# Kernel tuning notes

Hardware: AMD Instinct MI355X
Metric: run time of the kernel (lower is better)

## Reference

```python
import jax, jax.numpy as jnp
import numpy as np

L_OUTPUT = 1024  # SequenceDecoder l_output


def setup_inputs() -> dict:
    key = jax.random.key(0)
    k1, k2, k3 = jax.random.split(key, 3)
    B, L, D, DO = 16, 4096, 1024, 1024
    x = jax.random.normal(k1, (B, L, D), dtype=jnp.float32)
    # 0/1 padding-style mask; valid_length = mask.sum(axis=1)
    attention_mask = jax.random.randint(k2, (B, L), 0, 2, dtype=jnp.int32)
    # nn.Linear(d_model, d_output): weight (DO, D), bias (DO,)
    W = jax.random.normal(k3, (DO, D), dtype=jnp.float32) * (1.0 / np.sqrt(D))
    b = jnp.zeros((DO,), dtype=jnp.float32)
    return {"x": x, "attention_mask": attention_mask, "W": W, "b": b}


def _restrict_last(x, attention_mask, l_output):
    """Vectorized equivalent of the per-sample Python loop in mode='last':
    for each batch row i, take the LAST s_i = min(valid_len_i, l_output)
    elements of the full sequence, zero-padded at the tail to l_output.
    (When all s_i == l_output this matches x[:, -l_output:, :], which is the
    only case the original torch.stack-based loop handles without error.)"""
    B, L, D = x.shape
    valid = attention_mask.sum(axis=1)                    # (B,)
    s = jnp.minimum(valid, l_output)                      # (B,)
    j = jnp.arange(l_output)                              # (l_output,)
    idx = jnp.clip(L - s[:, None] + j[None, :], 0, L - 1) # (B, l_output)
    gathered = jnp.take_along_axis(x, idx[:, :, None], axis=1)  # (B, l_output, D)
    keep = (j[None, :] < s[:, None])[:, :, None]          # (B, l_output, 1)
    return jnp.where(keep, gathered, jnp.zeros((), dtype=x.dtype))


def reference(x, attention_mask, W, b):
    # mode='last' restrict, then output_transform = nn.Linear(d_model, d_output)
    restricted = _restrict_last(x, attention_mask, L_OUTPUT)  # (B, l_output, D)
    return jnp.einsum('bld,od->blo', restricted, W) + b       # (B, l_output, DO)
```

## Files before the change

kernel.cpp:

```cpp
#include <hip/hip_runtime.h>
#include <hip/hip_bf16.h>

#define L_SEQ   4096
#define D_IN    1024
#define N_BATCH 16
#define L_OUT   1024
#define D_OUT   1024
#define M_DIM   (N_BATCH * L_OUT)
#define K_DIM   D_IN

#define BM 256
#define BN 256
#define BK 32
#define NKT (K_DIM / BK)

typedef __attribute__((ext_vector_type(4))) float  f32x4;
typedef __attribute__((ext_vector_type(8))) __bf16 bf16x8;
typedef __attribute__((ext_vector_type(4))) __bf16 bf16x4;

#define WS_W_OFF 0u
#define WS_S_OFF (4u * 1024u * 1024u)

__global__ __launch_bounds__(256) void prep_kernel(
    const int*   __restrict__ mask,
    const float* __restrict__ W,
    int*    __restrict__ s_out,
    __bf16* __restrict__ wsW)
{
    const int t = threadIdx.x;
    if (blockIdx.x < 16) {
        const int b = blockIdx.x;
        const int* row = mask + (size_t)b * L_SEQ;
        int sum = 0;
#pragma unroll
        for (int i = 0; i < L_SEQ / 256; ++i) sum += row[t + i * 256];
#pragma unroll
        for (int off = 32; off > 0; off >>= 1) sum += __shfl_down(sum, off, 64);
        __shared__ int wsum[4];
        if ((t & 63) == 0) wsum[t >> 6] = sum;
        __syncthreads();
        if (t == 0) {
            int total = wsum[0] + wsum[1] + wsum[2] + wsum[3];
            s_out[b] = total < L_OUT ? total : L_OUT;
        }
    } else {
        const int n  = blockIdx.x - 16;
        const int e0 = t * 4;
        const int sl   = (e0 >> 3) & 3;
        const int dste = (e0 & ~31) | ((sl ^ ((n >> 1) & 3)) << 3) | (e0 & 7);
        const float* src = W + (size_t)n * D_IN + e0;
        f32x4 v = *(const f32x4*)src;
        bf16x4 o = {(__bf16)v.x, (__bf16)v.y, (__bf16)v.z, (__bf16)v.w};
        *(bf16x4*)(wsW + (size_t)n * K_DIM + dste) = o;
    }
}

__device__ __forceinline__ void gload16v(const void* g, void* l) {
    __builtin_amdgcn_global_load_lds(
        (const __attribute__((address_space(1))) void*)g,
        (__attribute__((address_space(3))) void*)l,
        16, 0, 0);
}

#define FENCE() asm volatile("" ::: "memory")

__global__ __launch_bounds__(512, 2) void gemm_kernel(
    const float*  __restrict__ x,
    const __bf16* __restrict__ Wb,
    const float*  __restrict__ bias,
    const int*    __restrict__ s_arr,
    float* __restrict__ out)
{
    __shared__ float  sAf[3][BM * BK];
    __shared__ __bf16 sB [2][BN * BK];

    const int t  = threadIdx.x;
    const int bx = blockIdx.x;
    const int vb = (bx & 7) * 32 + (bx >> 3);
    const int tile_n = vb & 3;
    const int tile_m = vb >> 2;
    const int m0 = tile_m * BM;
    const int n0 = tile_n * BN;
    const int lane = t & 63;
    const int wave = t >> 6;
    const int wm = wave & 3;
    const int wn = wave >> 2;

    const int bb = m0 >> 10;
    const int s  = s_arr[bb];
    const int jb = m0 & (L_OUT - 1);
    const float* xb = x + (size_t)bb * L_SEQ * D_IN;
    const int ascol = (((t & 7) ^ ((t >> 3) & 7)) * 4);
    const float* asrc[4];
    int  adst[4];
    int  arow[4];
#pragma unroll
    for (int r = 0; r < 4; ++r) {
        const int rr = 64 * r + (t >> 3);
        const int j  = jb + rr;
        const int xr = (j < s) ? (L_SEQ - s + j) : 0;
        asrc[r] = xb + (size_t)xr * D_IN + ascol;
        adst[r] = rr * BK + (t & 7) * 4;
        arow[r] = j;
    }
#define STAGE_A(abuf, kt_)                                                 \
    {                                                                      \
        _Pragma("unroll")                                                  \
        for (int r = 0; r < 4; ++r)                                        \
            gload16v(asrc[r] + (kt_) * BK, (abuf) + adst[r]);              \
    }

    const __bf16* Bg = Wb + (size_t)n0 * K_DIM;
    const int brow = t >> 2;
    const int bcol = (t & 3) * 8;
#define STAGE_B(buf, kt_)                                                  \
    {                                                                      \
        _Pragma("unroll")                                                  \
        for (int r = 0; r < 2; ++r) {                                      \
            const int row_ = 128 * r + brow;                               \
            gload16v(Bg + (size_t)row_ * K_DIM + (kt_) * BK + bcol,        \
                     &sB[buf][row_ * BK + bcol]);                          \
        }                                                                  \
    }

    const int fr = lane & 15;
    const int g4 = lane >> 4;

    float bias_v[8];
#pragma unroll
    for (int q = 0; q < 8; ++q)
        bias_v[q] = bias[n0 + wn * 128 + q * 16 + fr];

    bf16x8 aF[4], bBlo[4], bBhi[4];
    f32x4 acc[4][8];
#pragma unroll
    for (int i = 0; i < 4; ++i)
#pragma unroll
        for (int q = 0; q < 8; ++q) acc[i][q] = (f32x4){0.f, 0.f, 0.f, 0.f};

#define LOAD_A32(abuf)                                                     \
    {                                                                      \
        _Pragma("unroll")                                                  \
        for (int i = 0; i < 4; ++i) {                                      \
            const int R_ = wm * 64 + i * 16 + fr;                          \
            const float* rbase_ = (abuf) + R_ * BK;                        \
            f32x4 lo_ = *(const f32x4*)&rbase_[((2*g4)   ^ (R_ & 7)) * 4]; \
            f32x4 hi_ = *(const f32x4*)&rbase_[((2*g4+1) ^ (R_ & 7)) * 4]; \
            aF[i] = (bf16x8){(__bf16)lo_.x, (__bf16)lo_.y, (__bf16)lo_.z,  \
                             (__bf16)lo_.w, (__bf16)hi_.x, (__bf16)hi_.y,  \
                             (__bf16)hi_.z, (__bf16)hi_.w};                \
        }                                                                  \
    }

#define LOAD_B4(buf, qb, BB)                                               \
    {                                                                      \
        _Pragma("unroll")                                                  \
        for (int j = 0; j < 4; ++j) {                                      \
            const int RB_ = wn * 128 + ((qb) + j) * 16 + fr;               \
            BB[j] = *(const bf16x8*)                                       \
                &sB[buf][RB_ * BK + (g4 ^ ((RB_ >> 1) & 3)) * 8];          \
        }                                                                  \
    }

#define MFMA16(qb, BB)                                                     \
    {                                                                      \
        _Pragma("unroll")                                                  \
        for (int i = 0; i < 4; ++i)                                        \
            _Pragma("unroll")                                              \
            for (int j = 0; j < 4; ++j)                                    \
                acc[i][(qb) + j] =                                         \
                    __builtin_amdgcn_mfma_f32_16x16x32_bf16(               \
                        aF[i], BB[j], acc[i][(qb) + j], 0, 0, 0);          \
    }

    float* a0 = &sAf[0][0];
    float* a1 = &sAf[1][0];
    float* a2 = &sAf[2][0];

    STAGE_A(a0, 0);
    STAGE_B(0, 0);
    STAGE_A(a1, 1);

    for (int kt = 0; kt < NKT; ++kt) {
        const int cur = kt & 1;
        const int nxt = cur ^ 1;

        FENCE();
        if (kt == NKT - 1) asm volatile("s_waitcnt vmcnt(0)" ::: "memory");
        else               asm volatile("s_waitcnt vmcnt(4)" ::: "memory");
        __builtin_amdgcn_s_barrier();
        FENCE();
        if (s < L_OUT) {
#pragma unroll
            for (int r = 0; r < 4; ++r)
                if (arow[r] >= s)
                    *(f32x4*)&a0[adst[r]] = (f32x4){0.f, 0.f, 0.f, 0.f};
            __syncthreads();
        }
        LOAD_A32(a0);
        LOAD_B4(cur, 0, bBlo);
        if (kt + 1 < NKT) STAGE_B(nxt, kt + 1);
        __builtin_amdgcn_s_setprio(1);
        MFMA16(0, bBlo);
        __builtin_amdgcn_s_setprio(0);

        FENCE();
        __builtin_amdgcn_s_barrier();
        FENCE();
        LOAD_B4(cur, 4, bBhi);
        if (kt + 2 < NKT) STAGE_A(a2, kt + 2);
        __builtin_amdgcn_s_setprio(1);
        MFMA16(4, bBhi);
        __builtin_amdgcn_s_setprio(0);

        float* ta = a0; a0 = a1; a1 = a2; a2 = ta;
    }

    const int row0 = m0 + wm * 64 + (lane >> 4) * 4;
    const int col0 = n0 + wn * 128 + fr;
#pragma unroll
    for (int i = 0; i < 4; ++i)
#pragma unroll
        for (int q = 0; q < 8; ++q)
#pragma unroll
            for (int rr = 0; rr < 4; ++rr)
                out[(size_t)(row0 + i * 16 + rr) * D_OUT + (col0 + q * 16)] =
                    acc[i][q][rr] + bias_v[q];

#undef STAGE_A
#undef STAGE_B
#undef LOAD_A32
#undef LOAD_B4
#undef MFMA16
}

extern "C" void kernel_launch(void* const* d_in, const int* in_sizes, int n_in,
                              void* d_out, int out_size, void* d_ws, size_t ws_size,
                              hipStream_t stream) {
    const float* x    = (const float*)d_in[0];
    const int*   mask = (const int*)d_in[1];
    const float* W    = (const float*)d_in[2];
    const float* bias = (const float*)d_in[3];
    float*       out  = (float*)d_out;

    __bf16* wsW   = (__bf16*)((char*)d_ws + WS_W_OFF);
    int*    s_arr = (int*)((char*)d_ws + WS_S_OFF);

    prep_kernel<<<dim3(16 + D_OUT), dim3(256), 0, stream>>>(
        mask, W, s_arr, wsW);

    const int grid = (M_DIM / BM) * (D_OUT / BN);
    gemm_kernel<<<dim3(grid), dim3(512), 0, stream>>>(
        x, wsW, bias, s_arr, out);
}
```

Before: 51.79 us.

## Pre-pack weights into MFMA fragment order and load B directly to registers

The prep kernel now writes the bf16 weight matrix in a fragment-major layout that matches the per-lane MFMA B operand. The GEMM kernel then loads B fragments straight from global/L2 into registers, double-buffered across k-steps, instead of staging them through LDS. This drops the B LDS buffers and their LDS reads and frees LDS. The cost is more VGPRs for the two 8-fragment register buffers and per-wave global loads of B that are no longer shared through LDS. The wait count is raised to cover the extra outstanding loads, and the k loop is unrolled by two.

```diff
diff --git a/kernel.cpp b/kernel.cpp
--- a/kernel.cpp
+++ b/kernel.cpp
@@ -25,7 +25,7 @@
     const int*   __restrict__ mask,
     const float* __restrict__ W,
     int*    __restrict__ s_out,
-    __bf16* __restrict__ wsW)
+    __bf16* __restrict__ wsW2)
 {
     const int t = threadIdx.x;
     if (blockIdx.x < 16) {
@@ -45,13 +45,19 @@
         }
     } else {
         const int n  = blockIdx.x - 16;
-        const int e0 = t * 4;
-        const int sl   = (e0 >> 3) & 3;
-        const int dste = (e0 & ~31) | ((sl ^ ((n >> 1) & 3)) << 3) | (e0 & 7);
-        const float* src = W + (size_t)n * D_IN + e0;
-        f32x4 v = *(const f32x4*)src;
+        const int k0 = t * 4;
+        const int kt  = k0 >> 5;
+        const int g4p = (k0 >> 3) & 3;
+        const int e   = k0 & 7;
+        const int tn  = n >> 8;
+        const int wnp = (n >> 7) & 1;
+        const int f   = (n >> 4) & 7;
+        const int fr  = n & 15;
+        const size_t idx16 =
+            ((size_t)((tn * 2 + wnp) * 32 + kt)) * 512 + f * 64 + g4p * 16 + fr;
+        f32x4 v = *(const f32x4*)(W + (size_t)n * D_IN + k0);
         bf16x4 o = {(__bf16)v.x, (__bf16)v.y, (__bf16)v.z, (__bf16)v.w};
-        *(bf16x4*)(wsW + (size_t)n * K_DIM + dste) = o;
+        *(bf16x4*)((char*)wsW2 + idx16 * 16 + e * 2) = o;
     }
 }
 
@@ -66,13 +72,12 @@
 
 __global__ __launch_bounds__(512, 2) void gemm_kernel(
     const float*  __restrict__ x,
-    const __bf16* __restrict__ Wb,
+    const __bf16* __restrict__ Wb2,
     const float*  __restrict__ bias,
     const int*    __restrict__ s_arr,
     float* __restrict__ out)
 {
-    __shared__ float  sAf[3][BM * BK];
-    __shared__ __bf16 sB [2][BN * BK];
+    __shared__ float sAf[3][BM * BK];
 
     const int t  = threadIdx.x;
     const int bx = blockIdx.x;
@@ -110,17 +115,13 @@
             gload16v(asrc[r] + (kt_) * BK, (abuf) + adst[r]);              \
     }
 
-    const __bf16* Bg = Wb + (size_t)n0 * K_DIM;
-    const int brow = t >> 2;
-    const int bcol = (t & 3) * 8;
-#define STAGE_B(buf, kt_)                                                  \
-    {                                                                      \
-        _Pragma("unroll")                                                  \
-        for (int r = 0; r < 2; ++r) {                                      \
-            const int row_ = 128 * r + brow;                               \
-            gload16v(Bg + (size_t)row_ * K_DIM + (kt_) * BK + bcol,        \
-                     &sB[buf][row_ * BK + bcol]);                          \
-        }                                                                  \
+    const bf16x8* bgw = (const bf16x8*)Wb2 +
+        (size_t)(tile_n * 2 + wn) * 32 * 512 + lane;
+#define LOAD_BREG(BB, kt_)                                                 \
+    {                                                                      \
+        _Pragma("unroll")                                                  \
+        for (int f = 0; f < 8; ++f)                                        \
+            BB[f] = bgw[(kt_) * 512 + f * 64];                             \
     }
 
     const int fr = lane & 15;
@@ -131,7 +132,7 @@
     for (int q = 0; q < 8; ++q)
         bias_v[q] = bias[n0 + wn * 128 + q * 16 + fr];
 
-    bf16x8 aF[4], bBlo[4], bBhi[4];
+    bf16x8 aF[4], bBa[8], bBb[8];
     f32x4 acc[4][8];
 #pragma unroll
     for (int i = 0; i < 4; ++i)
@@ -152,25 +153,23 @@
         }                                                                  \
     }
 
-#define LOAD_B4(buf, qb, BB)                                               \
-    {                                                                      \
-        _Pragma("unroll")                                                  \
-        for (int j = 0; j < 4; ++j) {                                      \
-            const int RB_ = wn * 128 + ((qb) + j) * 16 + fr;               \
-            BB[j] = *(const bf16x8*)                                       \
-                &sB[buf][RB_ * BK + (g4 ^ ((RB_ >> 1) & 3)) * 8];          \
-        }                                                                  \
-    }
-
-#define MFMA16(qb, BB)                                                     \
+#define MFMA16LO(BB)                                                       \
     {                                                                      \
         _Pragma("unroll")                                                  \
         for (int i = 0; i < 4; ++i)                                        \
             _Pragma("unroll")                                              \
             for (int j = 0; j < 4; ++j)                                    \
-                acc[i][(qb) + j] =                                         \
-                    __builtin_amdgcn_mfma_f32_16x16x32_bf16(               \
-                        aF[i], BB[j], acc[i][(qb) + j], 0, 0, 0);          \
+                acc[i][j] = __builtin_amdgcn_mfma_f32_16x16x32_bf16(       \
+                    aF[i], BB[j], acc[i][j], 0, 0, 0);                     \
+    }
+#define MFMA16HI(BB)                                                       \
+    {                                                                      \
+        _Pragma("unroll")                                                  \
+        for (int i = 0; i < 4; ++i)                                        \
+            _Pragma("unroll")                                              \
+            for (int j = 0; j < 4; ++j)                                    \
+                acc[i][4 + j] = __builtin_amdgcn_mfma_f32_16x16x32_bf16(   \
+                    aF[i], BB[4 + j], acc[i][4 + j], 0, 0, 0);             \
     }
 
     float* a0 = &sAf[0][0];
@@ -178,42 +177,43 @@
     float* a2 = &sAf[2][0];
 
     STAGE_A(a0, 0);
-    STAGE_B(0, 0);
+    LOAD_BREG(bBa, 0);
     STAGE_A(a1, 1);
 
-    for (int kt = 0; kt < NKT; ++kt) {
-        const int cur = kt & 1;
-        const int nxt = cur ^ 1;
-
-        FENCE();
-        if (kt == NKT - 1) asm volatile("s_waitcnt vmcnt(0)" ::: "memory");
-        else               asm volatile("s_waitcnt vmcnt(4)" ::: "memory");
-        __builtin_amdgcn_s_barrier();
-        FENCE();
-        if (s < L_OUT) {
-#pragma unroll
-            for (int r = 0; r < 4; ++r)
-                if (arow[r] >= s)
-                    *(f32x4*)&a0[adst[r]] = (f32x4){0.f, 0.f, 0.f, 0.f};
-            __syncthreads();
-        }
-        LOAD_A32(a0);
-        LOAD_B4(cur, 0, bBlo);
-        if (kt + 1 < NKT) STAGE_B(nxt, kt + 1);
-        __builtin_amdgcn_s_setprio(1);
-        MFMA16(0, bBlo);
-        __builtin_amdgcn_s_setprio(0);
-
-        FENCE();
-        __builtin_amdgcn_s_barrier();
-        FENCE();
-        LOAD_B4(cur, 4, bBhi);
-        if (kt + 2 < NKT) STAGE_A(a2, kt + 2);
-        __builtin_amdgcn_s_setprio(1);
-        MFMA16(4, bBhi);
-        __builtin_amdgcn_s_setprio(0);
-
-        float* ta = a0; a0 = a1; a1 = a2; a2 = ta;
+#define BODY(KT, BBc, BBn)                                                 \
+    {                                                                      \
+        FENCE();                                                           \
+        if ((KT) == NKT - 1)                                               \
+            asm volatile("s_waitcnt vmcnt(0)" ::: "memory");               \
+        else                                                               \
+            asm volatile("s_waitcnt vmcnt(12)" ::: "memory");              \
+        __builtin_amdgcn_s_barrier();                                      \
+        FENCE();                                                           \
+        if (s < L_OUT) {                                                   \
+            _Pragma("unroll")                                              \
+            for (int r = 0; r < 4; ++r)                                    \
+                if (arow[r] >= s)                                          \
+                    *(f32x4*)&a0[adst[r]] = (f32x4){0.f, 0.f, 0.f, 0.f};   \
+            __syncthreads();                                               \
+        }                                                                  \
+        LOAD_A32(a0);                                                      \
+        if ((KT) + 1 < NKT) LOAD_BREG(BBn, (KT) + 1);                      \
+        __builtin_amdgcn_s_setprio(1);                                     \
+        MFMA16LO(BBc);                                                     \
+        __builtin_amdgcn_s_setprio(0);                                     \
+        FENCE();                                                           \
+        __builtin_amdgcn_s_barrier();                                      \
+        FENCE();                                                           \
+        if ((KT) + 2 < NKT) STAGE_A(a2, (KT) + 2);                         \
+        __builtin_amdgcn_s_setprio(1);                                     \
+        MFMA16HI(BBc);                                                     \
+        __builtin_amdgcn_s_setprio(0);                                     \
+        { float* ta = a0; a0 = a1; a1 = a2; a2 = ta; }                     \
+    }
+
+    for (int kt = 0; kt < NKT; kt += 2) {
+        BODY(kt,     bBa, bBb);
+        BODY(kt + 1, bBb, bBa);
     }
 
     const int row0 = m0 + wm * 64 + (lane >> 4) * 4;
@@ -228,10 +228,11 @@
                     acc[i][q][rr] + bias_v[q];
 
 #undef STAGE_A
-#undef STAGE_B
+#undef LOAD_BREG
 #undef LOAD_A32
-#undef LOAD_B4
-#undef MFMA16
+#undef MFMA16LO
+#undef MFMA16HI
+#undef BODY
 }
 
 extern "C" void kernel_launch(void* const* d_in, const int* in_sizes, int n_in,
@@ -243,13 +244,13 @@
     const float* bias = (const float*)d_in[3];
     float*       out  = (float*)d_out;
 
-    __bf16* wsW   = (__bf16*)((char*)d_ws + WS_W_OFF);
+    __bf16* wsW2  = (__bf16*)((char*)d_ws + WS_W_OFF);
     int*    s_arr = (int*)((char*)d_ws + WS_S_OFF);
 
     prep_kernel<<<dim3(16 + D_OUT), dim3(256), 0, stream>>>(
-        mask, W, s_arr, wsW);
+        mask, W, s_arr, wsW2);
 
     const int grid = (M_DIM / BM) * (D_OUT / BN);
     gemm_kernel<<<dim3(grid), dim3(512), 0, stream>>>(
-        x, wsW, bias, s_arr, out);
-}
+        x, wsW2, bias, s_arr, out);
+}
```

Measured after the change: 65.69 us. 26.8% more time.
